# Kernel tuning notes

Hardware: AMD Instinct MI355X
Metric: run time of the kernel (lower is better)

Reference implementation:

```python
import jax, jax.numpy as jnp
import numpy as np

NEG_SLOPE = 0.2  # LeakyReLU slope used in the torch module


def setup_inputs() -> dict:
    key = jax.random.key(0)
    k1, k2, k3, k4 = jax.random.split(key, 4)
    B, W, K, E = 32, 128, 128, 256  # E = 2*window_size (gatv2 doubles embed_dim)
    x = jax.random.normal(k1, (B, W, K), dtype=jnp.float32)
    lin_w = jax.random.normal(k2, (E, 2 * W), dtype=jnp.float32) * 0.05
    lin_b = jnp.zeros((E,), dtype=jnp.float32)
    a = jax.random.normal(k3, (E, 1), dtype=jnp.float32) * 0.1
    bias = jax.random.normal(k4, (K, K), dtype=jnp.float32) * 0.1
    return {"x": x, "lin_w": lin_w, "lin_b": lin_b, "a": a, "bias": bias}


def reference(x, lin_w, lin_b, a, bias):
    # x: [B, window, K] -> permute to [B, K, window]
    xp = jnp.transpose(x, (0, 2, 1))
    Wd = xp.shape[-1]
    # lin(concat(v_i, v_j)) = v_i @ Wl^T + v_j @ Wr^T + b, avoiding the
    # explicit repeat_interleave/repeat/cat of the torch code (same math).
    Wl, Wr = lin_w[:, :Wd], lin_w[:, Wd:]
    left = jnp.einsum('bkw,ew->bke', xp, Wl)   # [B, K, E]
    right = jnp.einsum('bkw,ew->bke', xp, Wr)  # [B, K, E]
    h = left[:, :, None, :] + right[:, None, :, :] + lin_b  # [B, K, K, E]
    h = jnp.where(h >= 0, h, NEG_SLOPE * h)  # LeakyReLU(0.2)
    e = jnp.einsum('bije,eo->bij', h, a)     # matmul with a, squeeze -> [B, K, K]
    e = e + bias                             # use_bias=True
    att = jax.nn.softmax(e, axis=2)          # dropout=0 / eval -> identity
    out = jax.nn.sigmoid(jnp.einsum('bij,bjw->biw', att, xp))  # [B, K, W]
    return jnp.transpose(out, (0, 2, 1))     # [B, window, K]
```

## Files before the change

kernel.cpp:

```cpp
#include <hip/hip_runtime.h>


typedef float v2f __attribute__((ext_vector_type(2)));
typedef float v4f __attribute__((ext_vector_type(4)));
typedef short bf16x8 __attribute__((ext_vector_type(8)));

#define WS_A6  2097152
#define WS_A4  (2097152 + 256)

__device__ __forceinline__ unsigned pack_bf16x2(float a, float b) {
    unsigned ua = __builtin_bit_cast(unsigned, a);
    unsigned ub = __builtin_bit_cast(unsigned, b);
    ua = (ua + 0x7FFFu + ((ua >> 16) & 1u)) >> 16;
    ub = (ub + 0x7FFFu + ((ub >> 16) & 1u)) >> 16;
    return ua | (ub << 16);
}

__global__ __launch_bounds__(256) void k_linear(
    const float* __restrict__ x, const float* __restrict__ lin_w,
    const float* __restrict__ lin_b, const float* __restrict__ a,
    float* __restrict__ ws)
{
    __shared__ unsigned short xT[64 * 136];
    __shared__ float Ps[64 * 68];

    const int t = threadIdx.x;
    const int b = blockIdx.x, rt = blockIdx.y, kt = blockIdx.z;
    const int r0 = rt * 64, k0 = kt * 64;
    const bool isL = (rt < 4);

    if (b == 0 && rt == 0 && kt == 0) {
        float av = a[t];
        ws[WS_A6 + t] = 0.6f * av;
        ws[WS_A4 + t] = 0.4f * av;
    }

    {
        const float* xg = x + b * 16384 + k0;
        #pragma unroll
        for (int q = 0; q < 4; ++q) {
            const int idx = t + q * 256;
            const int wp = idx >> 4;
            const int k4 = (idx & 15) << 2;
            const v4f r0v = *(const v4f*)(xg + (2 * wp) * 128 + k4);
            const v4f r1v = *(const v4f*)(xg + (2 * wp + 1) * 128 + k4);
            const int g   = wp >> 2;
            const int off = (2 * wp) & 7;
            #pragma unroll
            for (int u = 0; u < 4; ++u) {
                const int kk = k4 + u;
                const int gs = g ^ ((kk >> 3) & 15);
                *(unsigned*)&xT[kk * 136 + (gs << 3) + off] = pack_bf16x2(r0v[u], r1v[u]);
            }
        }
    }
    __syncthreads();

    const int l = t & 63, wave = t >> 6;
    const int lr = l & 15, lg = l >> 4;
    const int rr_a = wave * 16 + lr;
    const int r_g  = r0 + rr_a;
    const float* Arow = isL ? (lin_w + (size_t)r_g * 256)
                            : (lin_w + (size_t)(r_g - 256) * 256 + 128);
    bf16x8 af[4];
    #pragma unroll
    for (int kc = 0; kc < 4; ++kc) {
        const v4f a0 = *(const v4f*)(Arow + kc * 32 + lg * 8);
        const v4f a1 = *(const v4f*)(Arow + kc * 32 + lg * 8 + 4);
        unsigned p0 = pack_bf16x2(a0[0], a0[1]), p1 = pack_bf16x2(a0[2], a0[3]);
        unsigned p2 = pack_bf16x2(a1[0], a1[1]), p3 = pack_bf16x2(a1[2], a1[3]);
        af[kc] = __builtin_bit_cast(bf16x8, (uint4){p0, p1, p2, p3});
    }

    v4f acc[4];
    #pragma unroll
    for (int nf = 0; nf < 4; ++nf) acc[nf] = (v4f){0.f, 0.f, 0.f, 0.f};
    #pragma unroll
    for (int nf = 0; nf < 4; ++nf) {
        const int kk = nf * 16 + lr;
        const int vr = (kk >> 3) & 15;
        #pragma unroll
        for (int kc = 0; kc < 4; ++kc) {
            const bf16x8 bfv = *(const bf16x8*)&xT[kk * 136 + (((kc * 4 + lg) ^ vr) << 3)];
            acc[nf] = __builtin_amdgcn_mfma_f32_16x16x32_bf16(af[kc], bfv, acc[nf], 0, 0, 0);
        }
    }

    #pragma unroll
    for (int nf = 0; nf < 4; ++nf)
        #pragma unroll
        for (int j = 0; j < 4; ++j)
            Ps[(wave * 16 + lg * 4 + j) * 68 + nf * 16 + lr] = acc[nf][j];
    __syncthreads();

    #pragma unroll
    for (int q = 0; q < 4; ++q) {
        const int idx = t + q * 256;
        const int rr = idx >> 4, k4 = (idx & 15) << 2;
        const float lb = isL ? lin_b[r0 + rr] : 0.f;
        const v4f v = *(const v4f*)&Ps[rr * 68 + k4];
        float* dst = ws + ((size_t)(b * 512 + r0 + rr) * 128 + k0 + k4);
        *(v4f*)dst = (v4f){v[0] + lb, v[1] + lb, v[2] + lb, v[3] + lb};
    }
}

#define RS0 0
#define RS1 8192
#define LT  16384
#define A6  20480
#define A4  20736
#define DLR 20992
#define DRR 21120
#define ATT 22144

__global__ __launch_bounds__(512) void k_attn(
    const float* __restrict__ x, const float* __restrict__ bias,
    const float* __restrict__ ws, float* __restrict__ out)
{
    __shared__ __align__(16) float S[23232];

    const int t = threadIdx.x;
    const int b = blockIdx.x, it = blockIdx.y;
    const float* Pb = ws + (size_t)b * 65536;
    const float* Rsrc = Pb + 32768;

    v4f rx[4];
#define RLOAD(n_) do { const float* s_ = Rsrc + (n_) * 8192 + t * 4;  \
    _Pragma("unroll") for (int q = 0; q < 4; ++q)                     \
      rx[q] = *(const v4f*)(s_ + q * 2048); } while (0)

    RLOAD(0);

    {
        const float* Ls = Pb + it * 16;
        #pragma unroll
        for (int q = 0; q < 2; ++q) {
            const int idx = t + q * 512;
            const int e = idx >> 2, il4 = (idx & 3) * 4;
            *(v4f*)&S[LT + e * 16 + il4] = *(const v4f*)(Ls + e * 128 + il4);
        }
    }
    if (t < 256) S[A6 + t] = ws[WS_A6 + t];
    else         S[A4 + (t - 256)] = ws[WS_A4 + (t - 256)];

    const int l = t & 63, wv = t >> 6;
    const int jl = l & 31, il = l >> 5;
    const int j0e = jl * 4;

    float acc[8][4] = {};
    float dle[8] = {};
    float dre[4] = {};

    #pragma unroll 1
    for (int c = 0; c < 4; ++c) {
        const int cur = c & 1;
        {
            float* d_ = &S[RS0 + cur * 8192] + t * 4;
            #pragma unroll
            for (int q = 0; q < 4; ++q) *(v4f*)(d_ + q * 2048) = rx[q];
        }
        if (c < 3) RLOAD(c + 1);
        __syncthreads();

        const float* rs = &S[RS0 + cur * 8192];
        #pragma unroll
        for (int g = 0; g < 2; ++g) {
            const int er = wv * 8 + g * 4;
            const int eg = c * 64 + er;
            v4f rv[4], lA[4], lB[4];
            #pragma unroll
            for (int u = 0; u < 4; ++u) {
                rv[u] = *(const v4f*)&rs[(er + u) * 128 + j0e];
                lA[u] = *(const v4f*)&S[LT + (eg + u) * 16 + il * 8];
                lB[u] = *(const v4f*)&S[LT + (eg + u) * 16 + il * 8 + 4];
            }
            const v4f a6v = *(const v4f*)&S[A6 + eg];
            const v4f a4v = *(const v4f*)&S[A4 + eg];
            #pragma unroll
            for (int u = 0; u < 4; ++u) {
                const float a6u = a6v[u], a4u = a4v[u];
                #pragma unroll
                for (int q = 0; q < 4; ++q) {
                    const float la = lA[u][q], lb2 = lB[u][q];
                    dle[q]     = fmaf(a6u, la,  dle[q]);
                    dle[4 + q] = fmaf(a6u, lb2, dle[4 + q]);
                    #pragma unroll
                    for (int jj = 0; jj < 4; ++jj) {
                        const float r = rv[u][jj];
                        acc[q][jj]     = fmaf(a4u, fabsf(la  + r), acc[q][jj]);
                        acc[4 + q][jj] = fmaf(a4u, fabsf(lb2 + r), acc[4 + q][jj]);
                    }
                }
                #pragma unroll
                for (int jj = 0; jj < 4; ++jj)
                    dre[jj] = fmaf(a6u, rv[u][jj], dre[jj]);
            }
        }
    }
    __syncthreads();

    {
        float* red = &S[RS0];
        #pragma unroll
        for (int q = 0; q < 8; ++q)
            *(v4f*)&red[wv * 2048 + (il * 8 + q) * 128 + j0e] =
                (v4f){acc[q][0], acc[q][1], acc[q][2], acc[q][3]};
        if (jl == 0) {
            *(v4f*)&S[DLR + wv * 16 + il * 8]     = (v4f){dle[0], dle[1], dle[2], dle[3]};
            *(v4f*)&S[DLR + wv * 16 + il * 8 + 4] = (v4f){dle[4], dle[5], dle[6], dle[7]};
        }
        if (il == 0)
            *(v4f*)&S[DRR + wv * 128 + j0e] = (v4f){dre[0], dre[1], dre[2], dre[3]};
    }

    v4f xr[8];
    {
        const float* xg = x + b * 16384;
        #pragma unroll
        for (int q = 0; q < 4; ++q) {
            const int idx = t + q * 512;
            const int w = idx >> 4, j8 = (idx & 15) * 8;
            xr[2 * q]     = *(const v4f*)(xg + w * 128 + j8);
            xr[2 * q + 1] = *(const v4f*)(xg + w * 128 + j8 + 4);
        }
    }
    __syncthreads();

    {
        const int jps = t & 31, i = t >> 5;
        const int j0s = jps * 4;
        const int i0 = it * 16;
        const float* red = &S[RS0];
        v4f sm = *(const v4f*)&red[i * 128 + j0s];
        v4f drs = *(const v4f*)&S[DRR + j0s];
        float dls = S[DLR + i];
        #pragma unroll
        for (int es = 1; es < 8; ++es) {
            sm  += *(const v4f*)&red[es * 2048 + i * 128 + j0s];
            drs += *(const v4f*)&S[DRR + es * 128 + j0s];
            dls += S[DLR + es * 16 + i];
        }
        const v4f bi = *(const v4f*)(bias + (i0 + i) * 128 + j0s);
        float ev[4];
        #pragma unroll
        for (int jj = 0; jj < 4; ++jj) ev[jj] = sm[jj] + dls + drs[jj] + bi[jj];
        float m_ = fmaxf(fmaxf(ev[0], ev[1]), fmaxf(ev[2], ev[3]));
        #pragma unroll
        for (int d = 1; d <= 16; d <<= 1) m_ = fmaxf(m_, __shfl_xor(m_, d));
        float p0 = __expf(ev[0] - m_), p1 = __expf(ev[1] - m_);
        float p2 = __expf(ev[2] - m_), p3 = __expf(ev[3] - m_);
        float s_ = p0 + p1 + p2 + p3;
        #pragma unroll
        for (int d = 1; d <= 16; d <<= 1) s_ += __shfl_xor(s_, d);
        const float inv = 1.f / s_;
        unsigned* attu = (unsigned*)&S[ATT];
        attu[i * 68 + jps * 2]     = pack_bf16x2(p0 * inv, p1 * inv);
        attu[i * 68 + jps * 2 + 1] = pack_bf16x2(p2 * inv, p3 * inv);
    }
    __syncthreads();

    unsigned* ubf = (unsigned*)&S[RS1];
    #pragma unroll
    for (int q = 0; q < 4; ++q) {
        const int idx = t + q * 512;
        const int w = idx >> 4, jh = (idx & 15) * 4;
        const v4f x0 = xr[2 * q], x1 = xr[2 * q + 1];
        uint4 pk;
        pk.x = pack_bf16x2(x0[0], x0[1]);  pk.y = pack_bf16x2(x0[2], x0[3]);
        pk.z = pack_bf16x2(x1[0], x1[1]);  pk.w = pack_bf16x2(x1[2], x1[3]);
        *(uint4*)&ubf[w * 68 + jh] = pk;
    }
    __syncthreads();

    {
        const int lr = l & 15, lg = l >> 4;
        const int i0 = it * 16;
        const unsigned* attu = (const unsigned*)&S[ATT];
        bf16x8 paf[4];
        #pragma unroll
        for (int kc = 0; kc < 4; ++kc)
            paf[kc] = *(const bf16x8*)&attu[lr * 68 + kc * 16 + lg * 4];
        const int wrow = wv * 16 + lr;
        v4f pacc = (v4f){0.f, 0.f, 0.f, 0.f};
        #pragma unroll
        for (int kc = 0; kc < 4; ++kc) {
            const bf16x8 bv = *(const bf16x8*)&ubf[wrow * 68 + kc * 16 + lg * 4];
            pacc = __builtin_amdgcn_mfma_f32_16x16x32_bf16(paf[kc], bv, pacc, 0, 0, 0);
        }
        v4f r;
        r[0] = 1.f / (1.f + __expf(-pacc[0]));
        r[1] = 1.f / (1.f + __expf(-pacc[1]));
        r[2] = 1.f / (1.f + __expf(-pacc[2]));
        r[3] = 1.f / (1.f + __expf(-pacc[3]));
        *(v4f*)(out + (size_t)b * 16384 + wrow * 128 + i0 + lg * 4) = r;
    }
}

extern "C" void kernel_launch(void* const* d_in, const int* in_sizes, int n_in,
                              void* d_out, int out_size, void* d_ws, size_t ws_size,
                              hipStream_t stream) {
    const float* x     = (const float*)d_in[0];
    const float* lin_w = (const float*)d_in[1];
    const float* lin_b = (const float*)d_in[2];
    const float* a     = (const float*)d_in[3];
    const float* bias  = (const float*)d_in[4];
    float* ws  = (float*)d_ws;
    float* out = (float*)d_out;

    k_linear<<<dim3(32, 8, 2), 256, 0, stream>>>(x, lin_w, lin_b, a, ws);
    k_attn  <<<dim3(32, 8), 512, 0, stream>>>(x, bias, ws, out);
}
```

Measured before the change: 27.03 us.

## Fuse linear projection into attention kernel, computing projections per chunk in LDS

Merges the separate linear-projection kernel into the attention kernel. Each block now converts x to bf16 in shared memory, streams lin_w chunk by chunk through a register prefetch, and computes its needed left and right projections with MFMA inside the e-chunk loop. This removes the workspace round trip through global memory and one kernel launch. In exchange, each of the 8 i-tile blocks per batch redundantly recomputes the full right projection, and the loop carries more shared memory and more synchronisation.

Result: slower. 56.09 us (+107.5%).

```diff
diff --git a/kernel.cpp b/kernel.cpp
--- a/kernel.cpp
+++ b/kernel.cpp
@@ -4,9 +4,6 @@
 typedef float v2f __attribute__((ext_vector_type(2)));
 typedef float v4f __attribute__((ext_vector_type(4)));
 typedef short bf16x8 __attribute__((ext_vector_type(8)));
-
-#define WS_A6  2097152
-#define WS_A4  (2097152 + 256)
 
 __device__ __forceinline__ unsigned pack_bf16x2(float a, float b) {
     unsigned ua = __builtin_bit_cast(unsigned, a);
@@ -16,153 +13,140 @@
     return ua | (ub << 16);
 }
 
-__global__ __launch_bounds__(256) void k_linear(
+#define XT   0
+#define AS   8704
+#define RS   17152
+#define LTC  25600
+#define A6   26880
+#define A4   27136
+#define LBS  27392
+#define DLR  27648
+#define DRR  27776
+#define ATT  28800
+#define SSZ  29888
+
+__global__ __launch_bounds__(512) void k_fused(
     const float* __restrict__ x, const float* __restrict__ lin_w,
     const float* __restrict__ lin_b, const float* __restrict__ a,
-    float* __restrict__ ws)
+    const float* __restrict__ bias, float* __restrict__ out)
 {
-    __shared__ unsigned short xT[64 * 136];
-    __shared__ float Ps[64 * 68];
+    __shared__ __align__(16) float S[SSZ];
 
     const int t = threadIdx.x;
-    const int b = blockIdx.x, rt = blockIdx.y, kt = blockIdx.z;
-    const int r0 = rt * 64, k0 = kt * 64;
-    const bool isL = (rt < 4);
-
-    if (b == 0 && rt == 0 && kt == 0) {
-        float av = a[t];
-        ws[WS_A6 + t] = 0.6f * av;
-        ws[WS_A4 + t] = 0.4f * av;
-    }
-
-    {
-        const float* xg = x + b * 16384 + k0;
+    const int b = blockIdx.x, it = blockIdx.y;
+
+    unsigned short* xtu = (unsigned short*)&S[XT];
+    unsigned*       asu32 = (unsigned*)&S[AS];
+    const unsigned short* asu = (const unsigned short*)&S[AS];
+
+    v4f pre[8];
+#define WLOAD(c_) do {                                                       \
+    _Pragma("unroll") for (int q = 0; q < 8; ++q) {                          \
+        const int idx = t + q * 512;                                         \
+        const int rr = idx >> 6, cp = idx & 63;                              \
+        pre[q] = *(const v4f*)(lin_w + (size_t)((c_) * 64 + rr) * 256 + cp * 4); \
+    } } while (0)
+
+#define COMMIT() do {                                                        \
+    _Pragma("unroll") for (int q = 0; q < 8; ++q) {                          \
+        const int idx = t + q * 512;                                         \
+        const int rr = idx >> 6, cp = idx & 63;                              \
+        uint2 pk;                                                            \
+        pk.x = pack_bf16x2(pre[q][0], pre[q][1]);                            \
+        pk.y = pack_bf16x2(pre[q][2], pre[q][3]);                            \
+        *(uint2*)&asu32[rr * 132 + cp * 2] = pk; } } while (0)
+
+    WLOAD(0);
+
+    {
+        const float* xg = x + b * 16384;
         #pragma unroll
         for (int q = 0; q < 4; ++q) {
-            const int idx = t + q * 256;
-            const int wp = idx >> 4;
-            const int k4 = (idx & 15) << 2;
+            const int idx = t + q * 512;
+            const int wp = idx >> 5;
+            const int k4 = (idx & 31) << 2;
             const v4f r0v = *(const v4f*)(xg + (2 * wp) * 128 + k4);
             const v4f r1v = *(const v4f*)(xg + (2 * wp + 1) * 128 + k4);
             const int g   = wp >> 2;
             const int off = (2 * wp) & 7;
             #pragma unroll
             for (int u = 0; u < 4; ++u) {
-                const int kk = k4 + u;
-                const int gs = g ^ ((kk >> 3) & 15);
-                *(unsigned*)&xT[kk * 136 + (gs << 3) + off] = pack_bf16x2(r0v[u], r1v[u]);
-            }
-        }
-    }
+                const int k = k4 + u;
+                const int gs = g ^ ((k >> 3) & 15);
+                *(unsigned*)&xtu[k * 136 + (gs << 3) + off] = pack_bf16x2(r0v[u], r1v[u]);
+            }
+        }
+    }
+    if (t < 256) {
+        S[A6 + t]  = 0.6f * a[t];
+        S[A4 + t]  = 0.4f * a[t];
+        S[LBS + t] = lin_b[t];
+    }
+    COMMIT();
+    WLOAD(1);
     __syncthreads();
 
-    const int l = t & 63, wave = t >> 6;
+    const int l = t & 63, wv = t >> 6;
     const int lr = l & 15, lg = l >> 4;
-    const int rr_a = wave * 16 + lr;
-    const int r_g  = r0 + rr_a;
-    const float* Arow = isL ? (lin_w + (size_t)r_g * 256)
-                            : (lin_w + (size_t)(r_g - 256) * 256 + 128);
-    bf16x8 af[4];
-    #pragma unroll
-    for (int kc = 0; kc < 4; ++kc) {
-        const v4f a0 = *(const v4f*)(Arow + kc * 32 + lg * 8);
-        const v4f a1 = *(const v4f*)(Arow + kc * 32 + lg * 8 + 4);
-        unsigned p0 = pack_bf16x2(a0[0], a0[1]), p1 = pack_bf16x2(a0[2], a0[3]);
-        unsigned p2 = pack_bf16x2(a1[0], a1[1]), p3 = pack_bf16x2(a1[2], a1[3]);
-        af[kc] = __builtin_bit_cast(bf16x8, (uint4){p0, p1, p2, p3});
-    }
-
-    v4f acc[4];
-    #pragma unroll
-    for (int nf = 0; nf < 4; ++nf) acc[nf] = (v4f){0.f, 0.f, 0.f, 0.f};
-    #pragma unroll
-    for (int nf = 0; nf < 4; ++nf) {
-        const int kk = nf * 16 + lr;
-        const int vr = (kk >> 3) & 15;
-        #pragma unroll
-        for (int kc = 0; kc < 4; ++kc) {
-            const bf16x8 bfv = *(const bf16x8*)&xT[kk * 136 + (((kc * 4 + lg) ^ vr) << 3)];
-            acc[nf] = __builtin_amdgcn_mfma_f32_16x16x32_bf16(af[kc], bfv, acc[nf], 0, 0, 0);
-        }
-    }
-
-    #pragma unroll
-    for (int nf = 0; nf < 4; ++nf)
-        #pragma unroll
-        for (int j = 0; j < 4; ++j)
-            Ps[(wave * 16 + lg * 4 + j) * 68 + nf * 16 + lr] = acc[nf][j];
-    __syncthreads();
-
-    #pragma unroll
-    for (int q = 0; q < 4; ++q) {
-        const int idx = t + q * 256;
-        const int rr = idx >> 4, k4 = (idx & 15) << 2;
-        const float lb = isL ? lin_b[r0 + rr] : 0.f;
-        const v4f v = *(const v4f*)&Ps[rr * 68 + k4];
-        float* dst = ws + ((size_t)(b * 512 + r0 + rr) * 128 + k0 + k4);
-        *(v4f*)dst = (v4f){v[0] + lb, v[1] + lb, v[2] + lb, v[3] + lb};
-    }
-}
-
-#define RS0 0
-#define RS1 8192
-#define LT  16384
-#define A6  20480
-#define A4  20736
-#define DLR 20992
-#define DRR 21120
-#define ATT 22144
-
-__global__ __launch_bounds__(512) void k_attn(
-    const float* __restrict__ x, const float* __restrict__ bias,
-    const float* __restrict__ ws, float* __restrict__ out)
-{
-    __shared__ __align__(16) float S[23232];
-
-    const int t = threadIdx.x;
-    const int b = blockIdx.x, it = blockIdx.y;
-    const float* Pb = ws + (size_t)b * 65536;
-    const float* Rsrc = Pb + 32768;
-
-    v4f rx[4];
-#define RLOAD(n_) do { const float* s_ = Rsrc + (n_) * 8192 + t * 4;  \
-    _Pragma("unroll") for (int q = 0; q < 4; ++q)                     \
-      rx[q] = *(const v4f*)(s_ + q * 2048); } while (0)
-
-    RLOAD(0);
-
-    {
-        const float* Ls = Pb + it * 16;
-        #pragma unroll
-        for (int q = 0; q < 2; ++q) {
-            const int idx = t + q * 512;
-            const int e = idx >> 2, il4 = (idx & 3) * 4;
-            *(v4f*)&S[LT + e * 16 + il4] = *(const v4f*)(Ls + e * 128 + il4);
-        }
-    }
-    if (t < 256) S[A6 + t] = ws[WS_A6 + t];
-    else         S[A4 + (t - 256)] = ws[WS_A4 + (t - 256)];
-
-    const int l = t & 63, wv = t >> 6;
     const int jl = l & 31, il = l >> 5;
     const int j0e = jl * 4;
+    const int eg4 = wv >> 1;
+    const int jh  = wv & 1;
 
     float acc[8][4] = {};
     float dle[8] = {};
     float dre[4] = {};
+    v4f xr[8];
 
     #pragma unroll 1
     for (int c = 0; c < 4; ++c) {
-        const int cur = c & 1;
         {
-            float* d_ = &S[RS0 + cur * 8192] + t * 4;
-            #pragma unroll
-            for (int q = 0; q < 4; ++q) *(v4f*)(d_ + q * 2048) = rx[q];
-        }
-        if (c < 3) RLOAD(c + 1);
+            bf16x8 afR[4];
+            #pragma unroll
+            for (int kc = 0; kc < 4; ++kc)
+                afR[kc] = *(const bf16x8*)&asu[(eg4 * 16 + lr) * 264 + 128 + kc * 32 + lg * 8];
+            v4f aR[4];
+            #pragma unroll
+            for (int nf = 0; nf < 4; ++nf) aR[nf] = (v4f){0.f, 0.f, 0.f, 0.f};
+            #pragma unroll
+            for (int nf = 0; nf < 4; ++nf) {
+                const int row = jh * 64 + nf * 16 + lr;
+                const int vr = (row >> 3) & 15;
+                #pragma unroll
+                for (int kc = 0; kc < 4; ++kc) {
+                    const bf16x8 bv = *(const bf16x8*)&xtu[row * 136 + (((kc * 4 + lg) ^ vr) << 3)];
+                    aR[nf] = __builtin_amdgcn_mfma_f32_16x16x32_bf16(afR[kc], bv, aR[nf], 0, 0, 0);
+                }
+            }
+            #pragma unroll
+            for (int j = 0; j < 4; ++j) {
+                const int el = eg4 * 16 + lg * 4 + j;
+                #pragma unroll
+                for (int nf = 0; nf < 4; ++nf)
+                    S[RS + el * 132 + jh * 64 + nf * 16 + lr] = aR[nf][j];
+            }
+            if (jh == 0) {
+                bf16x8 afL[4];
+                #pragma unroll
+                for (int kc = 0; kc < 4; ++kc)
+                    afL[kc] = *(const bf16x8*)&asu[(eg4 * 16 + lr) * 264 + kc * 32 + lg * 8];
+                const int row = it * 16 + lr;
+                const int vr = (row >> 3) & 15;
+                v4f aL = (v4f){0.f, 0.f, 0.f, 0.f};
+                #pragma unroll
+                for (int kc = 0; kc < 4; ++kc) {
+                    const bf16x8 bv = *(const bf16x8*)&xtu[row * 136 + (((kc * 4 + lg) ^ vr) << 3)];
+                    aL = __builtin_amdgcn_mfma_f32_16x16x32_bf16(afL[kc], bv, aL, 0, 0, 0);
+                }
+                #pragma unroll
+                for (int j = 0; j < 4; ++j) {
+                    const int el = eg4 * 16 + lg * 4 + j;
+                    S[LTC + el * 20 + lr] = aL[j] + S[LBS + c * 64 + el];
+                }
+            }
+        }
         __syncthreads();
 
-        const float* rs = &S[RS0 + cur * 8192];
         #pragma unroll
         for (int g = 0; g < 2; ++g) {
             const int er = wv * 8 + g * 4;
@@ -170,9 +154,9 @@
             v4f rv[4], lA[4], lB[4];
             #pragma unroll
             for (int u = 0; u < 4; ++u) {
-                rv[u] = *(const v4f*)&rs[(er + u) * 128 + j0e];
-                lA[u] = *(const v4f*)&S[LT + (eg + u) * 16 + il * 8];
-                lB[u] = *(const v4f*)&S[LT + (eg + u) * 16 + il * 8 + 4];
+                rv[u] = *(const v4f*)&S[RS + (er + u) * 132 + j0e];
+                lA[u] = *(const v4f*)&S[LTC + (er + u) * 20 + il * 8];
+                lB[u] = *(const v4f*)&S[LTC + (er + u) * 20 + il * 8 + 4];
             }
             const v4f a6v = *(const v4f*)&S[A6 + eg];
             const v4f a4v = *(const v4f*)&S[A4 + eg];
@@ -196,11 +180,25 @@
                     dre[jj] = fmaf(a6u, rv[u][jj], dre[jj]);
             }
         }
-    }
-    __syncthreads();
-
-    {
-        float* red = &S[RS0];
+        if (c < 3) {
+            COMMIT();
+            if (c < 2) WLOAD(c + 2);
+            else {
+                const float* xg = x + b * 16384;
+                #pragma unroll
+                for (int q = 0; q < 4; ++q) {
+                    const int idx = t + q * 512;
+                    const int w = idx >> 4, j8 = (idx & 15) * 8;
+                    xr[2 * q]     = *(const v4f*)(xg + w * 128 + j8);
+                    xr[2 * q + 1] = *(const v4f*)(xg + w * 128 + j8 + 4);
+                }
+            }
+        }
+        __syncthreads();
+    }
+
+    {
+        float* red = &S[AS];
         #pragma unroll
         for (int q = 0; q < 8; ++q)
             *(v4f*)&red[wv * 2048 + (il * 8 + q) * 128 + j0e] =
@@ -212,25 +210,13 @@
         if (il == 0)
             *(v4f*)&S[DRR + wv * 128 + j0e] = (v4f){dre[0], dre[1], dre[2], dre[3]};
     }
-
-    v4f xr[8];
-    {
-        const float* xg = x + b * 16384;
-        #pragma unroll
-        for (int q = 0; q < 4; ++q) {
-            const int idx = t + q * 512;
-            const int w = idx >> 4, j8 = (idx & 15) * 8;
-            xr[2 * q]     = *(const v4f*)(xg + w * 128 + j8);
-            xr[2 * q + 1] = *(const v4f*)(xg + w * 128 + j8 + 4);
-        }
-    }
     __syncthreads();
 
     {
         const int jps = t & 31, i = t >> 5;
         const int j0s = jps * 4;
         const int i0 = it * 16;
-        const float* red = &S[RS0];
+        const float* red = &S[AS];
         v4f sm = *(const v4f*)&red[i * 128 + j0s];
         v4f drs = *(const v4f*)&S[DRR + j0s];
         float dls = S[DLR + i];
@@ -257,25 +243,25 @@
         attu[i * 68 + jps * 2]     = pack_bf16x2(p0 * inv, p1 * inv);
         attu[i * 68 + jps * 2 + 1] = pack_bf16x2(p2 * inv, p3 * inv);
     }
+    {
+        unsigned* ubf = (unsigned*)&S[XT];
+        #pragma unroll
+        for (int q = 0; q < 4; ++q) {
+            const int idx = t + q * 512;
+            const int w = idx >> 4, jhc = (idx & 15) * 4;
+            const v4f x0 = xr[2 * q], x1 = xr[2 * q + 1];
+            uint4 pk;
+            pk.x = pack_bf16x2(x0[0], x0[1]);  pk.y = pack_bf16x2(x0[2], x0[3]);
+            pk.z = pack_bf16x2(x1[0], x1[1]);  pk.w = pack_bf16x2(x1[2], x1[3]);
+            *(uint4*)&ubf[w * 68 + jhc] = pk;
+        }
+    }
     __syncthreads();
 
-    unsigned* ubf = (unsigned*)&S[RS1];
-    #pragma unroll
-    for (int q = 0; q < 4; ++q) {
-        const int idx = t + q * 512;
-        const int w = idx >> 4, jh = (idx & 15) * 4;
-        const v4f x0 = xr[2 * q], x1 = xr[2 * q + 1];
-        uint4 pk;
-        pk.x = pack_bf16x2(x0[0], x0[1]);  pk.y = pack_bf16x2(x0[2], x0[3]);
-        pk.z = pack_bf16x2(x1[0], x1[1]);  pk.w = pack_bf16x2(x1[2], x1[3]);
-        *(uint4*)&ubf[w * 68 + jh] = pk;
-    }
-    __syncthreads();
-
-    {
-        const int lr = l & 15, lg = l >> 4;
+    {
+        const unsigned* attu = (const unsigned*)&S[ATT];
+        const unsigned* ubf = (const unsigned*)&S[XT];
         const int i0 = it * 16;
-        const unsigned* attu = (const unsigned*)&S[ATT];
         bf16x8 paf[4];
         #pragma unroll
         for (int kc = 0; kc < 4; ++kc)
@@ -304,9 +290,8 @@
     const float* lin_b = (const float*)d_in[2];
     const float* a     = (const float*)d_in[3];
     const float* bias  = (const float*)d_in[4];
-    float* ws  = (float*)d_ws;
     float* out = (float*)d_out;
-
-    k_linear<<<dim3(32, 8, 2), 256, 0, stream>>>(x, lin_w, lin_b, a, ws);
-    k_attn  <<<dim3(32, 8), 512, 0, stream>>>(x, bias, ws, out);
+    (void)d_ws; (void)ws_size;
+
+    k_fused<<<dim3(32, 8), 512, 0, stream>>>(x, lin_w, lin_b, a, bias, out);
 }
```
